# Kernel optimization log

Measured on AMD Instinct MI355X. Metric: run time of the kernel, lower is better.

Reference implementation:

```python
import jax, jax.numpy as jnp
import numpy as np

# Grid: (batch, X, Y, Z); N sparse voxels, C channels, 3x3x3 depthwise kernel
GRID = (2, 256, 256, 256)
N = 600_000
C = 32
K = 3
R = K // 2  # kernel radius

# padded dims so shifted coords (by +/-R) stay in-range and keys stay unique
_PD = (GRID[0] + 2 * R, GRID[1] + 2 * R, GRID[2] + 2 * R, GRID[3] + 2 * R)


def _keys(coords):
    """Linearize [M,4] int coords (possibly offset by +/-R) into unique int64 keys
    whose sort order equals lexicographic order over (b, x, y, z)."""
    c = coords.astype(jnp.int64) + R
    return ((c[:, 0] * _PD[1] + c[:, 1]) * _PD[2] + c[:, 2]) * _PD[3] + c[:, 3]


def setup_inputs() -> dict:
    rng = np.random.default_rng(0)
    total = GRID[0] * GRID[1] * GRID[2] * GRID[3]
    lin = rng.choice(total, size=N, replace=False)  # unique voxel ids
    b = lin // (GRID[1] * GRID[2] * GRID[3])
    rem = lin % (GRID[1] * GRID[2] * GRID[3])
    x = rem // (GRID[2] * GRID[3])
    rem = rem % (GRID[2] * GRID[3])
    y = rem // GRID[3]
    z = rem % GRID[3]
    coords = jnp.asarray(np.stack([b, x, y, z], axis=1).astype(np.int32))

    k1, k2 = jax.random.split(jax.random.key(0))
    feats = jax.random.normal(k1, (N, C), dtype=jnp.float32)
    # per-channel depthwise kernel: C convs of shape 1->1 with K^3 taps
    weight = jax.random.normal(k2, (C, K ** 3), dtype=jnp.float32) * 0.1
    return {"feats": feats, "coords": coords, "weight": weight}


def reference(feats, coords, weight):
    # Sort points lexicographically by (b,x,y,z): this reproduces combine()'s
    # unique + lexsort ordering (stride=1 => output coords == input coords).
    keys = _keys(coords)
    order = jnp.argsort(keys)
    skeys = keys[order]          # [N] sorted keys
    sfeats = feats[order]        # [N, C]
    out_coords = coords[order]   # [N, 4]
    n = skeys.shape[0]

    out = jnp.zeros_like(sfeats)
    k = 0
    for dx in range(-R, R + 1):
        for dy in range(-R, R + 1):
            for dz in range(-R, R + 1):
                off = jnp.array([0, dx, dy, dz], dtype=jnp.int32)
                q = _keys(out_coords + off[None, :])       # neighbor keys [N]
                pos = jnp.searchsorted(skeys, q)
                posc = jnp.clip(pos, 0, n - 1)
                match = skeys[posc] == q                   # neighbor exists?
                g = jnp.where(match[:, None], sfeats[posc], 0.0)  # [N, C]
                out = out + g * weight[None, :, k]         # depthwise tap k
                k += 1
    return out, out_coords
```

## Files before the change

### kernel.cpp

```cpp
#include <hip/hip_runtime.h>

#define NPTS_C 32
#define NTAPS 27
#define KEY_WORDS (1u << 20)
#define SCAN_BLOCKS 1024

typedef float f32x4 __attribute__((ext_vector_type(4)));

__device__ __forceinline__ unsigned make_key(int b, int x, int y, int z) {
    return ((((unsigned)b << 8 | (unsigned)x) << 8 | (unsigned)y) << 8) | (unsigned)z;
}

__global__ void k_scatter_bits(const int4* __restrict__ coords, unsigned* __restrict__ bitmask, int n) {
    int i = blockIdx.x * blockDim.x + threadIdx.x;
    if (i >= n) return;
    int4 co = coords[i];
    unsigned key = make_key(co.x, co.y, co.z, co.w);
    atomicOr(&bitmask[key >> 5], 1u << (key & 31u));
}

__global__ void k_popc_sums(const uint4* __restrict__ bm4, unsigned* __restrict__ blockSums) {
    int t = threadIdx.x;
    uint4 w = bm4[blockIdx.x * 256 + t];
    unsigned s = __popc(w.x) + __popc(w.y) + __popc(w.z) + __popc(w.w);
    for (int off = 32; off > 0; off >>= 1) s += __shfl_down(s, off, 64);
    __shared__ unsigned wsum[4];
    if ((t & 63) == 0) wsum[t >> 6] = s;
    __syncthreads();
    if (t == 0) blockSums[blockIdx.x] = wsum[0] + wsum[1] + wsum[2] + wsum[3];
}

__global__ void k_build_combined(const uint4* __restrict__ bm4, const unsigned* __restrict__ blockSums,
                                 uint4* __restrict__ combined4) {
    int t = threadIdx.x, lane = t & 63;
    __shared__ unsigned preW[4];
    __shared__ unsigned wsum[4];

    unsigned pre = 0;
    for (int i = t; i < blockIdx.x; i += 256) pre += blockSums[i];
    for (int off = 32; off > 0; off >>= 1) pre += __shfl_down(pre, off, 64);
    if (lane == 0) preW[t >> 6] = pre;
    __syncthreads();
    unsigned blockBase = preW[0] + preW[1] + preW[2] + preW[3];

    int gw = blockIdx.x * 256 + t;
    uint4 w = bm4[gw];
    unsigned p0 = __popc(w.x), p1 = __popc(w.y), p2 = __popc(w.z), p3 = __popc(w.w);
    unsigned s = p0 + p1 + p2 + p3;
    unsigned incl = s;
    for (int off = 1; off < 64; off <<= 1) {
        unsigned u = __shfl_up(incl, off, 64);
        if (lane >= off) incl += u;
    }
    if (lane == 63) wsum[t >> 6] = incl;
    __syncthreads();
    unsigned waveBase = 0;
    int wv = t >> 6;
    for (int i = 0; i < wv; i++) waveBase += wsum[i];
    unsigned excl = blockBase + waveBase + incl - s;
    uint4 a; a.x = w.x; a.y = excl;           a.z = w.y; a.w = excl + p0;
    uint4 b; b.x = w.z; b.y = excl + p0 + p1; b.z = w.w; b.w = excl + p0 + p1 + p2;
    combined4[gw * 2 + 0] = a;
    combined4[gw * 2 + 1] = b;
}

__device__ __forceinline__ unsigned rank_of(unsigned key, const uint2* __restrict__ combined) {
    uint2 cw = combined[key >> 5];
    unsigned bit = key & 31u;
    return cw.y + __popc(cw.x & ((1u << bit) - 1u));
}

__global__ __launch_bounds__(256) void k_scatter_feats(const float* __restrict__ feats,
                                                       const int4* __restrict__ coords,
                                                       const uint2* __restrict__ combined,
                                                       float* __restrict__ sfeats,
                                                       float* __restrict__ outCoordsF, int n) {
    int q = threadIdx.x & 7;
    int i0 = blockIdx.x * 64 + (threadIdx.x >> 3);
    int i1 = i0 + 32;
    bool vA = i0 < n, vB = i1 < n;

    int4 coA, coB;
    float4 fA, fB;
    if (vA) coA = coords[i0];
    if (vB) coB = coords[i1];
    if (vA) fA = ((const float4*)(feats + (size_t)i0 * NPTS_C))[q];
    if (vB) fB = ((const float4*)(feats + (size_t)i1 * NPTS_C))[q];

    unsigned rA = 0, rB = 0;
    if (vA) rA = rank_of(make_key(coA.x, coA.y, coA.z, coA.w), combined);
    if (vB) rB = rank_of(make_key(coB.x, coB.y, coB.z, coB.w), combined);

    if (vA) {
        ((float4*)(sfeats + (size_t)rA * NPTS_C))[q] = fA;
        if (q == 0) {
            float4 fc; fc.x = (float)coA.x; fc.y = (float)coA.y; fc.z = (float)coA.z; fc.w = (float)coA.w;
            ((float4*)outCoordsF)[rA] = fc;
        }
    }
    if (vB) {
        ((float4*)(sfeats + (size_t)rB * NPTS_C))[q] = fB;
        if (q == 0) {
            float4 fc; fc.x = (float)coB.x; fc.y = (float)coB.y; fc.z = (float)coB.z; fc.w = (float)coB.w;
            ((float4*)outCoordsF)[rB] = fc;
        }
    }
}

__global__ __launch_bounds__(256) void k_conv_sorted4(const float* __restrict__ sfeats,
                                                      const float* __restrict__ weight,
                                                      const float* __restrict__ outCoordsF,
                                                      const uint2* __restrict__ combined,
                                                      float* __restrict__ out, int n) {
    __shared__ float4 swT4[NTAPS * 9];
    __shared__ int ldsN[8][4][28];

    int t = threadIdx.x;
    for (int idx = t; idx < NTAPS * 8; idx += 256) {
        int kk = idx >> 3, q = idx & 7;
        float4 w4;
        w4.x = weight[(4 * q + 0) * NTAPS + kk];
        w4.y = weight[(4 * q + 1) * NTAPS + kk];
        w4.z = weight[(4 * q + 2) * NTAPS + kk];
        w4.w = weight[(4 * q + 3) * NTAPS + kk];
        swT4[kk * 9 + q] = w4;
    }

    int nwg = gridDim.x;
    int q8 = nwg >> 3, r8 = nwg & 7;
    int xcd = blockIdx.x & 7, idx8 = blockIdx.x >> 3;
    int bid = (xcd < r8) ? xcd * (q8 + 1) + idx8
                         : r8 * (q8 + 1) + (xcd - r8) * q8 + idx8;

    int gi = t >> 5, l = t & 31;
    bool hi = (t & 32) != 0;
    int p0 = (bid * 8 + gi) * 4;
    int cluster = l >> 3, q = l & 7;

    int dxl = l / 9 - 1, dyl = (l % 9) / 3 - 1, dzl = l % 3 - 1;
    int jl = l / 3;
    int pbx = l / 3 - 1, pby = l % 3 - 1;

    int cbA[4], cxA[4], cyA[4], czA[4];
    #pragma unroll
    for (int r = 0; r < 4; r++) {
        int pc = min(p0 + r, n - 1);
        float4 cf = ((const float4*)outCoordsF)[pc];
        cbA[r] = (int)cf.x; cxA[r] = (int)cf.y; cyA[r] = (int)cf.z; czA[r] = (int)cf.w;
    }

    uint2 cwA[4];
    #pragma unroll
    for (int r = 0; r < 4; r++) {
        uint2 cw; cw.x = 0u; cw.y = 0u;
        if (l < 9) {
            int xj = cxA[r] + pbx, yj = cyA[r] + pby;
            if ((unsigned)xj < 256u && (unsigned)yj < 256u)
                cw = combined[make_key(cbA[r], xj, yj, czA[r]) >> 5];
        }
        cwA[r] = cw;
    }

    uint2 spA[4];
    #pragma unroll
    for (int r = 0; r < 4; r++) {
        int x = cxA[r] + dxl, y = cyA[r] + dyl, z = czA[r] + dzl;
        bool ok = (l < NTAPS) && (l != 13) &&
                  (unsigned)x < 256u && (unsigned)y < 256u && (unsigned)z < 256u;
        bool sp = ok && ((z >> 5) != (czA[r] >> 5));
        uint2 t2; t2.x = 0u; t2.y = 0u;
        if (sp) t2 = combined[make_key(cbA[r], x, y, z) >> 5];
        spA[r] = t2;
    }

    int pm = p0 + cluster;
    float4 fc_c; fc_c.x = fc_c.y = fc_c.z = fc_c.w = 0.0f;
    if (pm < n) fc_c = ((const float4*)(sfeats + (size_t)pm * NPTS_C))[q];

    unsigned mk[4];
    #pragma unroll
    for (int r = 0; r < 4; r++) {
        unsigned bb = __shfl(cwA[r].x, jl, 32);
        unsigned pp = __shfl(cwA[r].y, jl, 32);
        int x = cxA[r] + dxl, y = cyA[r] + dyl, z = czA[r] + dzl;
        bool ok = (l < NTAPS) && (l != 13) &&
                  (unsigned)x < 256u && (unsigned)y < 256u && (unsigned)z < 256u;
        bool sp = ok && ((z >> 5) != (czA[r] >> 5));
        if (sp) { bb = spA[r].x; pp = spA[r].y; }
        int nidx = -1;
        if (ok) {
            unsigned keyk = make_key(cbA[r], x, y, z);
            unsigned bit = keyk & 31u;
            if ((bb >> bit) & 1u)
                nidx = (int)(pp + __popc(bb & ((1u << bit) - 1u)));
        }
        unsigned long long bal = __ballot(nidx >= 0);
        mk[r] = hi ? (unsigned)(bal >> 32) : (unsigned)bal;
        if (l < NTAPS) ldsN[gi][r][l] = nidx;
    }
    __syncthreads();

    float4 acc; acc.x = acc.y = acc.z = acc.w = 0.0f;
    if (pm < n) {
        float4 w4 = swT4[13 * 9 + q];
        acc.x = fc_c.x * w4.x; acc.y = fc_c.y * w4.y; acc.z = fc_c.z * w4.z; acc.w = fc_c.w * w4.w;
    }

    unsigned m = mk[cluster];
    while (m) {
        int kk = __ffs(m) - 1; m &= m - 1;
        int g = ldsN[gi][cluster][kk];
        float4 f = ((const float4*)(sfeats + (size_t)g * NPTS_C))[q];
        float4 w4 = swT4[kk * 9 + q];
        acc.x += f.x * w4.x; acc.y += f.y * w4.y; acc.z += f.z * w4.z; acc.w += f.w * w4.w;
    }
    if (pm < n) {
        f32x4 v; v.x = acc.x; v.y = acc.y; v.z = acc.z; v.w = acc.w;
        f32x4* dst = (f32x4*)(out + (size_t)pm * NPTS_C);
        __builtin_nontemporal_store(v, &dst[q]);
    }
}

__global__ void k_scatter_rank(const int4* __restrict__ coords, const uint2* __restrict__ combined,
                               int* __restrict__ origOf, int n) {
    int i = blockIdx.x * blockDim.x + threadIdx.x;
    if (i >= n) return;
    int4 co = coords[i];
    unsigned r = rank_of(make_key(co.x, co.y, co.z, co.w), combined);
    origOf[r] = i;
}

__device__ __forceinline__ int resolve_tap(int cb, int cx, int cy, int cz, int k,
                                           const uint2* __restrict__ combined) {
    int dx = k / 9 - 1, dy = (k % 9) / 3 - 1, dz = k % 3 - 1;
    int x = cx + dx, y = cy + dy, z = cz + dz;
    bool valid = (k < NTAPS) && ((unsigned)x < 256u) && ((unsigned)y < 256u) && ((unsigned)z < 256u);
    uint2 cw; cw.x = 0u; cw.y = 0u;
    if (k < 9) {
        int dxj = k / 3 - 1, dyj = k % 3 - 1;
        int xj = cx + dxj, yj = cy + dyj;
        if ((unsigned)xj < 256u && (unsigned)yj < 256u)
            cw = combined[make_key(cb, xj, yj, cz) >> 5];
    }
    int j = k / 3;
    unsigned bb = __shfl(cw.x, j, 32);
    unsigned pp = __shfl(cw.y, j, 32);
    int nidx = -1;
    if (valid) {
        unsigned keyk = make_key(cb, x, y, z);
        if ((z >> 5) != (cz >> 5)) {
            uint2 t2 = combined[keyk >> 5];
            bb = t2.x; pp = t2.y;
        }
        unsigned bit = keyk & 31u;
        if ((bb >> bit) & 1u)
            nidx = (int)(pp + __popc(bb & ((1u << bit) - 1u)));
    }
    return nidx;
}

__global__ __launch_bounds__(256) void k_conv_indirect(const float* __restrict__ feats, const float* __restrict__ weight,
                                                       const int4* __restrict__ coords,
                                                       const uint2* __restrict__ combined,
                                                       const int* __restrict__ origOf,
                                                       float* __restrict__ out, float* __restrict__ outCoordsF, int n) {
    __shared__ float swT[NTAPS * 32];
    for (int idx = threadIdx.x; idx < NTAPS * 32; idx += 256) {
        int kk = idx >> 5, cc = idx & 31;
        swT[idx] = weight[cc * NTAPS + kk];
    }
    __syncthreads();

    int p = blockIdx.x * 8 + (threadIdx.x >> 5);
    int c = threadIdx.x & 31;
    if (p >= n) return;

    int orig = origOf[p];
    int4 co = coords[orig];
    if (c == 0) {
        float4 f; f.x = (float)co.x; f.y = (float)co.y; f.z = (float)co.z; f.w = (float)co.w;
        ((float4*)outCoordsF)[p] = f;
    }

    int nidx0 = resolve_tap(co.x, co.y, co.z, co.w, c, combined);
    int nidx = (nidx0 >= 0) ? origOf[nidx0] : -1;

    unsigned long long full = __ballot(nidx >= 0);
    unsigned mymask = (threadIdx.x & 32) ? (unsigned)(full >> 32) : (unsigned)full;

    float acc = 0.0f;
    while (mymask) {
        int kk = __ffs(mymask) - 1;
        mymask &= mymask - 1;
        int g = __shfl(nidx, kk, 32);
        acc += feats[(size_t)g * NPTS_C + c] * swT[kk * 32 + c];
    }
    out[(size_t)p * NPTS_C + c] = acc;
}

extern "C" void kernel_launch(void* const* d_in, const int* in_sizes, int n_in,
                              void* d_out, int out_size, void* d_ws, size_t ws_size,
                              hipStream_t stream) {
    const float* feats  = (const float*)d_in[0];
    const int4*  coords = (const int4*)d_in[1];
    const float* weight = (const float*)d_in[2];
    const int n = in_sizes[1] / 4;

    float* out        = (float*)d_out;
    float* outCoordsF = (float*)d_out + n * NPTS_C;

    char* ws = (char*)d_ws;
    unsigned* bitmask   = (unsigned*)ws;
    uint2*    combined  = (uint2*)(ws + (size_t)KEY_WORDS * 4);
    unsigned* blockSums = (unsigned*)(ws + (size_t)KEY_WORDS * 12);
    char*     rest      = ws + (size_t)KEY_WORDS * 12 + 4096;

    size_t need_big = (size_t)KEY_WORDS * 12 + 4096 + (size_t)n * NPTS_C * 4;
    bool big = ws_size >= need_big;

    (void)hipMemsetAsync(bitmask, 0, (size_t)KEY_WORDS * 4, stream);

    int tb = 256;
    k_scatter_bits<<<(n + tb - 1) / tb, tb, 0, stream>>>(coords, bitmask, n);
    k_popc_sums<<<SCAN_BLOCKS, 256, 0, stream>>>((const uint4*)bitmask, blockSums);
    k_build_combined<<<SCAN_BLOCKS, 256, 0, stream>>>((const uint4*)bitmask, blockSums, (uint4*)combined);

    if (big) {
        float* sfeats = (float*)rest;
        k_scatter_feats<<<(n + 63) / 64, 256, 0, stream>>>(feats, coords, combined,
                                                           sfeats, outCoordsF, n);
        k_conv_sorted4<<<(n + 31) / 32, 256, 0, stream>>>(sfeats, weight, outCoordsF, combined, out, n);
    } else {
        int* origOf = (int*)bitmask;
        k_scatter_rank<<<(n + tb - 1) / tb, tb, 0, stream>>>(coords, combined, origOf, n);
        k_conv_indirect<<<(n + 7) / 8, 256, 0, stream>>>(feats, weight, coords, combined, origOf, out, outCoordsF, n);
    }
}
```

Before: 237.8 us.

## Process eight points per 32-lane group with direct per-tap bitmask lookups

The sorted convolution kernel now handles eight points per 32-lane group instead of four, and launches half as many blocks. Each lane loads the bitmask/prefix word for its own tap directly, replacing the shared x-y column loads plus shuffles and the separate cross-word loads. Neighbor indices are passed through register shuffles instead of an LDS table. This trades more registers and eight scattered lookups per lane for fewer LDS writes, less launch overhead and more independent loads in flight, at some risk of lower occupancy.

```diff
diff --git a/kernel.cpp b/kernel.cpp
--- a/kernel.cpp
+++ b/kernel.cpp
@@ -9,6 +9,13 @@
 
 __device__ __forceinline__ unsigned make_key(int b, int x, int y, int z) {
     return ((((unsigned)b << 8 | (unsigned)x) << 8 | (unsigned)y) << 8) | (unsigned)z;
+}
+
+__device__ __forceinline__ unsigned sel4u(int c, unsigned a0, unsigned a1, unsigned a2, unsigned a3) {
+    return c == 0 ? a0 : c == 1 ? a1 : c == 2 ? a2 : a3;
+}
+__device__ __forceinline__ int sel4i(int c, int a0, int a1, int a2, int a3) {
+    return c == 0 ? a0 : c == 1 ? a1 : c == 2 ? a2 : a3;
 }
 
 __global__ void k_scatter_bits(const int4* __restrict__ coords, unsigned* __restrict__ bitmask, int n) {
@@ -107,13 +114,12 @@
     }
 }
 
-__global__ __launch_bounds__(256) void k_conv_sorted4(const float* __restrict__ sfeats,
+__global__ __launch_bounds__(256) void k_conv_sorted8(const float* __restrict__ sfeats,
                                                       const float* __restrict__ weight,
                                                       const float* __restrict__ outCoordsF,
                                                       const uint2* __restrict__ combined,
                                                       float* __restrict__ out, int n) {
     __shared__ float4 swT4[NTAPS * 9];
-    __shared__ int ldsN[8][4][28];
 
     int t = threadIdx.x;
     for (int idx = t; idx < NTAPS * 8; idx += 256) {
@@ -134,90 +140,88 @@
 
     int gi = t >> 5, l = t & 31;
     bool hi = (t & 32) != 0;
-    int p0 = (bid * 8 + gi) * 4;
+    int p0 = (bid * 8 + gi) * 8;
     int cluster = l >> 3, q = l & 7;
 
     int dxl = l / 9 - 1, dyl = (l % 9) / 3 - 1, dzl = l % 3 - 1;
-    int jl = l / 3;
-    int pbx = l / 3 - 1, pby = l % 3 - 1;
-
-    int cbA[4], cxA[4], cyA[4], czA[4];
+    bool lane_tap = (l < NTAPS) && (l != 13);
+
+    int pmA = p0 + cluster, pmB = p0 + 4 + cluster;
+    float4 fcA; fcA.x = fcA.y = fcA.z = fcA.w = 0.0f;
+    float4 fcB = fcA;
+    if (pmA < n) fcA = ((const float4*)(sfeats + (size_t)pmA * NPTS_C))[q];
+    if (pmB < n) fcB = ((const float4*)(sfeats + (size_t)pmB * NPTS_C))[q];
+
+    int4 co[8];
     #pragma unroll
-    for (int r = 0; r < 4; r++) {
+    for (int r = 0; r < 8; r++) {
         int pc = min(p0 + r, n - 1);
         float4 cf = ((const float4*)outCoordsF)[pc];
-        cbA[r] = (int)cf.x; cxA[r] = (int)cf.y; cyA[r] = (int)cf.z; czA[r] = (int)cf.w;
-    }
-
-    uint2 cwA[4];
+        co[r].x = (int)cf.x; co[r].y = (int)cf.y; co[r].z = (int)cf.z; co[r].w = (int)cf.w;
+    }
+
+    unsigned key[8]; bool ok[8]; uint2 cw[8];
     #pragma unroll
-    for (int r = 0; r < 4; r++) {
-        uint2 cw; cw.x = 0u; cw.y = 0u;
-        if (l < 9) {
-            int xj = cxA[r] + pbx, yj = cyA[r] + pby;
-            if ((unsigned)xj < 256u && (unsigned)yj < 256u)
-                cw = combined[make_key(cbA[r], xj, yj, czA[r]) >> 5];
-        }
-        cwA[r] = cw;
-    }
-
-    uint2 spA[4];
+    for (int r = 0; r < 8; r++) {
+        int x = co[r].y + dxl, y = co[r].z + dyl, z = co[r].w + dzl;
+        ok[r] = lane_tap && (unsigned)x < 256u && (unsigned)y < 256u && (unsigned)z < 256u;
+        key[r] = make_key(co[r].x, x & 255, y & 255, z & 255);
+        cw[r] = combined[ok[r] ? (key[r] >> 5) : 0u];
+    }
+
+    int nn[8]; unsigned mk[8];
     #pragma unroll
-    for (int r = 0; r < 4; r++) {
-        int x = cxA[r] + dxl, y = cyA[r] + dyl, z = czA[r] + dzl;
-        bool ok = (l < NTAPS) && (l != 13) &&
-                  (unsigned)x < 256u && (unsigned)y < 256u && (unsigned)z < 256u;
-        bool sp = ok && ((z >> 5) != (czA[r] >> 5));
-        uint2 t2; t2.x = 0u; t2.y = 0u;
-        if (sp) t2 = combined[make_key(cbA[r], x, y, z) >> 5];
-        spA[r] = t2;
-    }
-
-    int pm = p0 + cluster;
-    float4 fc_c; fc_c.x = fc_c.y = fc_c.z = fc_c.w = 0.0f;
-    if (pm < n) fc_c = ((const float4*)(sfeats + (size_t)pm * NPTS_C))[q];
-
-    unsigned mk[4];
-    #pragma unroll
-    for (int r = 0; r < 4; r++) {
-        unsigned bb = __shfl(cwA[r].x, jl, 32);
-        unsigned pp = __shfl(cwA[r].y, jl, 32);
-        int x = cxA[r] + dxl, y = cyA[r] + dyl, z = czA[r] + dzl;
-        bool ok = (l < NTAPS) && (l != 13) &&
-                  (unsigned)x < 256u && (unsigned)y < 256u && (unsigned)z < 256u;
-        bool sp = ok && ((z >> 5) != (czA[r] >> 5));
-        if (sp) { bb = spA[r].x; pp = spA[r].y; }
-        int nidx = -1;
-        if (ok) {
-            unsigned keyk = make_key(cbA[r], x, y, z);
-            unsigned bit = keyk & 31u;
-            if ((bb >> bit) & 1u)
-                nidx = (int)(pp + __popc(bb & ((1u << bit) - 1u)));
-        }
-        unsigned long long bal = __ballot(nidx >= 0);
+    for (int r = 0; r < 8; r++) {
+        unsigned bit = key[r] & 31u;
+        int nid = -1;
+        if (ok[r] && ((cw[r].x >> bit) & 1u))
+            nid = (int)(cw[r].y + __popc(cw[r].x & ((1u << bit) - 1u)));
+        nn[r] = nid;
+        unsigned long long bal = __ballot(nid >= 0);
         mk[r] = hi ? (unsigned)(bal >> 32) : (unsigned)bal;
-        if (l < NTAPS) ldsN[gi][r][l] = nidx;
-    }
-    __syncthreads();
-
-    float4 acc; acc.x = acc.y = acc.z = acc.w = 0.0f;
-    if (pm < n) {
-        float4 w4 = swT4[13 * 9 + q];
-        acc.x = fc_c.x * w4.x; acc.y = fc_c.y * w4.y; acc.z = fc_c.z * w4.z; acc.w = fc_c.w * w4.w;
-    }
-
-    unsigned m = mk[cluster];
-    while (m) {
-        int kk = __ffs(m) - 1; m &= m - 1;
-        int g = ldsN[gi][cluster][kk];
+    }
+    __syncthreads();
+
+    float4 accA; accA.x = accA.y = accA.z = accA.w = 0.0f;
+    float4 accB = accA;
+    {
+        float4 w13 = swT4[13 * 9 + q];
+        if (pmA < n) { accA.x = fcA.x * w13.x; accA.y = fcA.y * w13.y; accA.z = fcA.z * w13.z; accA.w = fcA.w * w13.w; }
+        if (pmB < n) { accB.x = fcB.x * w13.x; accB.y = fcB.y * w13.y; accB.z = fcB.z * w13.z; accB.w = fcB.w * w13.w; }
+    }
+
+    unsigned mA = sel4u(cluster, mk[0], mk[1], mk[2], mk[3]);
+    unsigned mB = sel4u(cluster, mk[4], mk[5], mk[6], mk[7]);
+    while (mA) {
+        int kk = __ffs(mA) - 1; mA &= mA - 1;
+        int g0 = __shfl(nn[0], kk, 32);
+        int g1 = __shfl(nn[1], kk, 32);
+        int g2 = __shfl(nn[2], kk, 32);
+        int g3 = __shfl(nn[3], kk, 32);
+        int g = sel4i(cluster, g0, g1, g2, g3);
         float4 f = ((const float4*)(sfeats + (size_t)g * NPTS_C))[q];
         float4 w4 = swT4[kk * 9 + q];
-        acc.x += f.x * w4.x; acc.y += f.y * w4.y; acc.z += f.z * w4.z; acc.w += f.w * w4.w;
-    }
-    if (pm < n) {
-        f32x4 v; v.x = acc.x; v.y = acc.y; v.z = acc.z; v.w = acc.w;
-        f32x4* dst = (f32x4*)(out + (size_t)pm * NPTS_C);
-        __builtin_nontemporal_store(v, &dst[q]);
+        accA.x += f.x * w4.x; accA.y += f.y * w4.y; accA.z += f.z * w4.z; accA.w += f.w * w4.w;
+    }
+    while (mB) {
+        int kk = __ffs(mB) - 1; mB &= mB - 1;
+        int g4 = __shfl(nn[4], kk, 32);
+        int g5 = __shfl(nn[5], kk, 32);
+        int g6 = __shfl(nn[6], kk, 32);
+        int g7 = __shfl(nn[7], kk, 32);
+        int g = sel4i(cluster, g4, g5, g6, g7);
+        float4 f = ((const float4*)(sfeats + (size_t)g * NPTS_C))[q];
+        float4 w4 = swT4[kk * 9 + q];
+        accB.x += f.x * w4.x; accB.y += f.y * w4.y; accB.z += f.z * w4.z; accB.w += f.w * w4.w;
+    }
+
+    if (pmA < n) {
+        f32x4 v; v.x = accA.x; v.y = accA.y; v.z = accA.z; v.w = accA.w;
+        __builtin_nontemporal_store(v, &((f32x4*)(out + (size_t)pmA * NPTS_C))[q]);
+    }
+    if (pmB < n) {
+        f32x4 v; v.x = accB.x; v.y = accB.y; v.z = accB.z; v.w = accB.w;
+        __builtin_nontemporal_store(v, &((f32x4*)(out + (size_t)pmB * NPTS_C))[q]);
     }
 }
 
@@ -329,7 +333,7 @@
         float* sfeats = (float*)rest;
         k_scatter_feats<<<(n + 63) / 64, 256, 0, stream>>>(feats, coords, combined,
                                                            sfeats, outCoordsF, n);
-        k_conv_sorted4<<<(n + 31) / 32, 256, 0, stream>>>(sfeats, weight, outCoordsF, combined, out, n);
+        k_conv_sorted8<<<(n + 63) / 64, 256, 0, stream>>>(sfeats, weight, outCoordsF, combined, out, n);
     } else {
         int* origOf = (int*)bitmask;
         k_scatter_rank<<<(n + tb - 1) / tb, tb, 0, stream>>>(coords, combined, origOf, n);
```

Measured after the change: 229.2 us. 3.6% less time.
